# Kernel tuning notes

Measured on AMD Instinct MI355X. Metric: run time of the kernel, lower is better.

Reference implementation:

```python
import jax, jax.numpy as jnp
import numpy as np

# Scaled-up constants (GRID_SIZE=96)
AFFINE_HIDDEN_DIM = 128
ATTENTION_DIM = 256
EMBEDDING_DIM = 512
MAX_CONTRAST = 1.8
RANGE_SIZE = 4
NUM_RANGE_BLOCKS = 13824   # (96//4)**3
NUM_DOMAIN_BLOCKS = 1728   # (96//8)**3
SOFTMAX_TEMPERATURE = 0.25


def setup_inputs() -> dict:
    key = jax.random.key(0)
    ks = jax.random.split(key, 17)
    E, A, H = EMBEDDING_DIM, ATTENTION_DIM, AFFINE_HIDDEN_DIM
    NR, ND = NUM_RANGE_BLOCKS, NUM_DOMAIN_BLOCKS
    s_lin = 1.0 / np.sqrt(E)  # torch Linear default init scale
    return {
        "pooled_domains": jax.random.normal(ks[0], (ND, RANGE_SIZE, RANGE_SIZE, RANGE_SIZE), jnp.float32),
        "range_latents": jax.random.normal(ks[1], (NR, E), jnp.float32),
        "domain_latents": jax.random.normal(ks[2], (ND, E), jnp.float32),
        "range_positional": jax.random.normal(ks[3], (NR, E), jnp.float32),
        "domain_positional": jax.random.normal(ks[4], (ND, E), jnp.float32),
        "W_rproj": jax.random.normal(ks[5], (E, A), jnp.float32) * s_lin,
        "b_rproj": jax.random.normal(ks[6], (A,), jnp.float32) * s_lin,
        "W_dproj": jax.random.normal(ks[7], (E, A), jnp.float32) * s_lin,
        "b_dproj": jax.random.normal(ks[8], (A,), jnp.float32) * s_lin,
        "W_rcon": jax.random.normal(ks[9], (E, H), jnp.float32) * s_lin,
        "b_rcon": jax.random.normal(ks[10], (H,), jnp.float32) * s_lin,
        "W_dcon": jax.random.normal(ks[11], (E, H), jnp.float32) * s_lin,
        "b_dcon": jax.random.normal(ks[12], (H,), jnp.float32) * s_lin,
        "W_roff": jax.random.normal(ks[13], (E, H), jnp.float32) * s_lin,
        "b_roff": jax.random.normal(ks[14], (H,), jnp.float32) * s_lin,
        "W_doff": jax.random.normal(ks[15], (E, H), jnp.float32) * s_lin,
        "b_doff": jax.random.normal(ks[16], (H,), jnp.float32) * s_lin,
    }


def reference(pooled_domains, range_latents, domain_latents,
              range_positional, domain_positional,
              W_rproj, b_rproj, W_dproj, b_dproj,
              W_rcon, b_rcon, W_dcon, b_dcon,
              W_roff, b_roff, W_doff, b_doff):
    range_base = range_latents + range_positional      # [NR, E]
    domain_base = domain_latents + domain_positional   # [ND, E]

    range_repr = range_base @ W_rproj + b_rproj        # [NR, A]
    domain_repr = domain_base @ W_dproj + b_dproj      # [ND, A]

    inv_sqrt_h = 1.0 / np.sqrt(AFFINE_HIDDEN_DIM).astype(np.float32)
    range_con = range_base @ W_rcon + b_rcon           # [NR, H]
    domain_con = domain_base @ W_dcon + b_dcon         # [ND, H]
    contrast = jnp.tanh((range_con @ domain_con.T) * inv_sqrt_h) * MAX_CONTRAST  # [NR, ND]

    range_off = range_base @ W_roff + b_roff
    domain_off = domain_base @ W_doff + b_doff
    offset = jnp.tanh((range_off @ domain_off.T) * inv_sqrt_h)  # [NR, ND]

    scale = 1.0 / (np.sqrt(ATTENTION_DIM).astype(np.float32) * SOFTMAX_TEMPERATURE)
    logits = (range_repr @ domain_repr.T) * scale      # [NR, ND]
    weights = jax.nn.softmax(logits, axis=-1)          # [NR, ND]

    domain_flat = pooled_domains.reshape(NUM_DOMAIN_BLOCKS, -1)   # [ND, 64]
    scaled_domains = (weights * contrast) @ domain_flat           # [NR, 64]
    offset_effective = jnp.sum(weights * offset, axis=1, keepdims=True)  # [NR, 1]
    decoded = (scaled_domains + offset_effective).reshape(-1, RANGE_SIZE, RANGE_SIZE, RANGE_SIZE)
    return decoded
```

## Files before the change

### kernel.cpp

```cpp
#include <hip/hip_runtime.h>
#include <stdint.h>

#define NRB 13824
#define NDB 1728
#define EDIM 512
#define SPLIT 18
#define DPB (NDB/SPLIT)
#define TILES (DPB/32)

typedef __attribute__((ext_vector_type(8))) _Float16 h8;
typedef __attribute__((ext_vector_type(4))) float f4;

typedef __attribute__((address_space(3))) void lds_void;
typedef const __attribute__((address_space(1))) void gbl_void;

#define MFMA(a,b,c) __builtin_amdgcn_mfma_f32_16x16x32_f16(a,b,c,0,0,0)

static __device__ __forceinline__ ushort f2h(float f){
  union { _Float16 h; ushort u; } cv;
  cv.h = (_Float16)f;
  return cv.u;
}

static __device__ __forceinline__ float tanh_fast(float x){
  float ax = __builtin_fabsf(x);
  float t = __builtin_amdgcn_exp2f(ax * -2.8853900817779268f);
  float r = (1.0f - t) * __builtin_amdgcn_rcpf(1.0f + t);
  return __builtin_copysignf(r, x);
}

__global__ void prep_kernel(
    const float* __restrict__ pooled,
    const float* __restrict__ rlat, const float* __restrict__ dlat,
    const float* __restrict__ rpos, const float* __restrict__ dpos,
    const float* __restrict__ Wrp, const float* __restrict__ brp,
    const float* __restrict__ Wdp, const float* __restrict__ bdp,
    const float* __restrict__ Wrc, const float* __restrict__ brc,
    const float* __restrict__ Wdc, const float* __restrict__ bdc,
    const float* __restrict__ Wro, const float* __restrict__ bro,
    const float* __restrict__ Wdo2, const float* __restrict__ bdo2,
    ushort* __restrict__ rb, ushort* __restrict__ db,
    ushort* __restrict__ Wr_t, ushort* __restrict__ Wd_t,
    float* __restrict__ br_c, float* __restrict__ bd_c,
    ushort* __restrict__ dflt)
{
  const int NRE = NRB*EDIM, NDE = NDB*EDIM;
  int i0 = blockIdx.x*blockDim.x + threadIdx.x;
  int stride = gridDim.x*blockDim.x;
  for (int i=i0; i<NRE; i+=stride) rb[i] = f2h(rlat[i]+rpos[i]);
  for (int i=i0; i<NDE; i+=stride) db[i] = f2h(dlat[i]+dpos[i]);
  for (int i=i0; i<512*512; i+=stride){
    int n = i>>9, k = i&511;
    float vr = (n<256) ? Wrp[k*256+n] : ((n<384) ? Wrc[k*128+(n-256)] : Wro[k*128+(n-384)]);
    float vd = (n<256) ? Wdp[k*256+n] : ((n<384) ? Wdc[k*128+(n-256)] : Wdo2[k*128+(n-384)]);
    Wr_t[i] = f2h(vr); Wd_t[i] = f2h(vd);
  }
  for (int i=i0; i<512; i+=stride){
    br_c[i] = (i<256) ? brp[i] : ((i<384) ? brc[i-256] : bro[i-384]);
    bd_c[i] = (i<256) ? bdp[i] : ((i<384) ? bdc[i-256] : bdo2[i-384]);
  }
  for (int i=i0; i<64*NDB; i+=stride){
    int c = i/NDB, d = i - c*NDB;
    dflt[i] = f2h(pooled[d*64+c]);
  }
}

__global__ __launch_bounds__(256) void gemm_feats(
    const ushort* __restrict__ A,
    const ushort* __restrict__ Bt,
    const float* __restrict__ bias,
    ushort* __restrict__ C,
    int M)
{
  __shared__ ushort As[128*32];
  __shared__ ushort Bs[128*32];
  const int tid = threadIdx.x;
  const int lane = tid & 63;
  const int wave = tid >> 6;
  const int l15 = lane & 15;
  const int lhi = lane >> 4;
  const int row0 = blockIdx.x * 128;
  const int col0 = blockIdx.y * 128;
  const int wr = (wave>>1)*64;
  const int wc = (wave&1)*64;

  f4 acc[4][4] = {};
  char* Ab = (char*)As; char* Bb = (char*)Bs;

  for (int k0=0; k0<EDIM; k0+=32){
    __syncthreads();
    #pragma unroll
    for (int c=0;c<2;c++){
      int L = (tid + c*256)*16;
      int r = L>>6;
      int kb = L&63;
      int kbs = kb ^ ((r&3)<<4);
      int ra = row0 + r; if (ra > M-1) ra = M-1;
      const ushort* srcA = A + (size_t)ra*EDIM + k0 + (kbs>>1);
      const ushort* srcB = Bt + (size_t)(col0+r)*EDIM + k0 + (kbs>>1);
      __builtin_amdgcn_global_load_lds((gbl_void*)srcA, (lds_void*)(Ab + L), 16, 0, 0);
      __builtin_amdgcn_global_load_lds((gbl_void*)srcB, (lds_void*)(Bb + L), 16, 0, 0);
    }
    __syncthreads();
    h8 af[4], bf[4];
    #pragma unroll
    for (int i=0;i<4;i++){
      int rowa = wr + i*16 + l15;
      af[i] = *(const h8*)(Ab + (((rowa*64) + lhi*16) ^ ((rowa&3)<<4)));
      int rowb = wc + i*16 + l15;
      bf[i] = *(const h8*)(Bb + (((rowb*64) + lhi*16) ^ ((rowb&3)<<4)));
    }
    #pragma unroll
    for (int i=0;i<4;i++){
      #pragma unroll
      for (int j=0;j<4;j++){
        acc[i][j] = MFMA(af[i], bf[j], acc[i][j]);
      }
    }
  }

  #pragma unroll
  for (int j=0;j<4;j++){
    int col = col0 + wc + j*16 + l15;
    float bv = bias[col];
    #pragma unroll
    for (int i=0;i<4;i++){
      #pragma unroll
      for (int r=0;r<4;r++){
        int row = row0 + wr + i*16 + lhi*4 + r;
        if (row < M) C[(size_t)row*EDIM + col] = f2h(acc[i][j][r] + bv);
      }
    }
  }
}

__global__ __launch_bounds__(512, 2) void attn_kernel(
    const ushort* __restrict__ rfeat,
    const ushort* __restrict__ dfeat,
    const ushort* __restrict__ dflt,
    ushort* __restrict__ accbuf,
    float* __restrict__ mlbuf)
{
  __shared__ ushort DF[DPB*512];
  __shared__ ushort PT[8][16*32];

  const int tid  = threadIdx.x;
  const int wave = tid >> 6;
  const int lane = tid & 63;
  const int l15  = lane & 15;
  const int lhi  = lane >> 4;
  const int wrow = blockIdx.x*128 + wave*16;
  const int by   = blockIdx.y;
  const int dbase = by * DPB;

  constexpr float CL = 0.25f * 1.4426950408889634f;
  constexpr float CH = 0.08838834764831845f;

  char* DFb = (char*)DF;
  char* PTb = (char*)PT[wave];

  #pragma unroll
  for (int c=0;c<12;c++){
    int id = tid + c*512;
    int dom = id >> 6;
    h8 v = *(const h8*)(dfeat + (size_t)(dbase+dom)*EDIM + (id&63)*8);
    *(h8*)(DFb + ((id*16) ^ ((dom&7)<<4))) = v;
  }

  h8 q[16];
  {
    const ushort* qr = rfeat + (size_t)(wrow + l15)*EDIM + lhi*8;
    #pragma unroll
    for (int c=0;c<16;c++) q[c] = *(const h8*)(qr + c*32);
  }

  f4 acc[4] = {};
  float m2[4], lsum[4] = {0.f,0.f,0.f,0.f}, offa[4] = {0.f,0.f,0.f,0.f};
  #pragma unroll
  for (int r=0;r<4;r++) m2[r] = -1e30f;

  __syncthreads();

  for (int t=0; t<TILES; ++t){
    const int d0 = dbase + t*32;
    const int dloc = t*32;

    f4 SL[2] = {}, SC[2] = {}, SO[2] = {};
    #pragma unroll
    for (int ct=0; ct<2; ++ct){
      const int dom = dloc + ct*16 + l15;
      const int swz = (dom&7)<<4;
      const int base = dom*1024 + lhi*16;
      #pragma unroll
      for (int c=0;c<8;c++){
        h8 b = *(const h8*)(DFb + ((base + c*64) ^ swz));
        SL[ct] = MFMA(q[c], b, SL[ct]);
      }
      #pragma unroll
      for (int c=8;c<12;c++){
        h8 b = *(const h8*)(DFb + ((base + c*64) ^ swz));
        SC[ct] = MFMA(q[c], b, SC[ct]);
      }
      #pragma unroll
      for (int c=12;c<16;c++){
        h8 b = *(const h8*)(DFb + ((base + c*64) ^ swz));
        SO[ct] = MFMA(q[c], b, SO[ct]);
      }
    }

    #pragma unroll
    for (int r=0;r<4;r++){
      float la = SL[0][r]*CL;
      float lb = SL[1][r]*CL;
      float tm = fmaxf(la, lb);
      tm = fmaxf(tm, __shfl_xor(tm, 1, 64));
      tm = fmaxf(tm, __shfl_xor(tm, 2, 64));
      tm = fmaxf(tm, __shfl_xor(tm, 4, 64));
      tm = fmaxf(tm, __shfl_xor(tm, 8, 64));
      float mn = fmaxf(m2[r], tm);
      float al = __builtin_amdgcn_exp2f(m2[r] - mn);
      m2[r] = mn;
      lsum[r] *= al; offa[r] *= al;
      acc[0][r] *= al; acc[1][r] *= al; acc[2][r] *= al; acc[3][r] *= al;
      float pa = __builtin_amdgcn_exp2f(la - mn);
      float pb = __builtin_amdgcn_exp2f(lb - mn);
      lsum[r] += pa + pb;
      float ca = tanh_fast(SC[0][r]*CH)*1.8f;
      float cb = tanh_fast(SC[1][r]*CH)*1.8f;
      float oa = tanh_fast(SO[0][r]*CH);
      float ob = tanh_fast(SO[1][r]*CH);
      offa[r] += pa*oa + pb*ob;
      int row = lhi*4 + r;
      int rswz = (row&3)<<4;
      *(ushort*)(PTb + ((row*64 + l15*2) ^ rswz))      = f2h(pa*ca);
      *(ushort*)(PTb + ((row*64 + 32 + l15*2) ^ rswz)) = f2h(pb*cb);
    }

    __builtin_amdgcn_sched_barrier(0);

    {
      h8 pa = *(const h8*)(PTb + ((l15*64 + lhi*16) ^ ((l15&3)<<4)));
      #pragma unroll
      for (int nt=0; nt<4; nt++){
        int n = nt*16 + l15;
        h8 vb = *(const h8*)(dflt + (size_t)n*NDB + d0 + lhi*8);
        acc[nt] = MFMA(pa, vb, acc[nt]);
      }
    }

    __builtin_amdgcn_sched_barrier(0);
  }

  #pragma unroll
  for (int r=0;r<4;r++){
    float ls = lsum[r], oa = offa[r];
    ls += __shfl_xor(ls,1,64); ls += __shfl_xor(ls,2,64);
    ls += __shfl_xor(ls,4,64); ls += __shfl_xor(ls,8,64);
    oa += __shfl_xor(oa,1,64); oa += __shfl_xor(oa,2,64);
    oa += __shfl_xor(oa,4,64); oa += __shfl_xor(oa,8,64);
    int row = wrow + lhi*4 + r;
    size_t base = ((size_t)by*NRB + row)*64;
    #pragma unroll
    for (int nt=0; nt<4; nt++){
      accbuf[base + nt*16 + l15] = f2h(acc[nt][r]);
    }
    if (l15 == 0){
      size_t mo = ((size_t)by*NRB + row)*4;
      mlbuf[mo+0] = m2[r];
      mlbuf[mo+1] = ls;
      mlbuf[mo+2] = oa;
    }
  }
}

__global__ __launch_bounds__(256) void combine_kernel(
    const ushort* __restrict__ accbuf,
    const float* __restrict__ mlbuf,
    float* __restrict__ out)
{
  __shared__ float wS[64][SPLIT];
  __shared__ float c0S[64], iTS[64];
  const int rb = blockIdx.x;
  const int tid = threadIdx.x;

  if (tid < 64){
    int row = rb*64 + tid;
    float M = -1e30f;
    float m[SPLIT], l[SPLIT], o[SPLIT];
    #pragma unroll
    for (int s=0;s<SPLIT;s++){
      size_t off = ((size_t)s*NRB + row)*4;
      m[s]=mlbuf[off]; l[s]=mlbuf[off+1]; o[s]=mlbuf[off+2];
      M = fmaxf(M, m[s]);
    }
    float T=0.f, C=0.f;
    #pragma unroll
    for (int s=0;s<SPLIT;s++){
      float w = __builtin_amdgcn_exp2f(m[s]-M);
      wS[tid][s]=w; T += l[s]*w; C += o[s]*w;
    }
    c0S[tid]=C; iTS[tid]=1.0f/T;
  }
  __syncthreads();

  const int row_l = tid>>2;
  const int cb = (tid&3)*16;
  const int row = rb*64 + row_l;
  float res[16] = {};
  #pragma unroll
  for (int s=0;s<SPLIT;s++){
    float w = wS[row_l][s];
    const ushort* ap = accbuf + ((size_t)s*NRB + row)*64 + cb;
    h8 v0 = *(const h8*)(ap);
    h8 v1 = *(const h8*)(ap + 8);
    #pragma unroll
    for (int j=0;j<8;j++){
      res[j]   += (float)v0[j]*w;
      res[j+8] += (float)v1[j]*w;
    }
  }
  float C = c0S[row_l], iT = iTS[row_l];
  #pragma unroll
  for (int j=0;j<16;j++) out[(size_t)row*64 + cb + j] = (res[j]+C)*iT;
}

extern "C" void kernel_launch(void* const* d_in, const int* in_sizes, int n_in,
                              void* d_out, int out_size, void* d_ws, size_t ws_size,
                              hipStream_t stream) {
  const float* pooled = (const float*)d_in[0];
  const float* rlat   = (const float*)d_in[1];
  const float* dlat   = (const float*)d_in[2];
  const float* rpos   = (const float*)d_in[3];
  const float* dpos   = (const float*)d_in[4];
  const float* Wrp    = (const float*)d_in[5];
  const float* brp    = (const float*)d_in[6];
  const float* Wdp    = (const float*)d_in[7];
  const float* bdp    = (const float*)d_in[8];
  const float* Wrc    = (const float*)d_in[9];
  const float* brc    = (const float*)d_in[10];
  const float* Wdc    = (const float*)d_in[11];
  const float* bdc    = (const float*)d_in[12];
  const float* Wro    = (const float*)d_in[13];
  const float* bro    = (const float*)d_in[14];
  const float* Wdo2   = (const float*)d_in[15];
  const float* bdo2   = (const float*)d_in[16];

  char* ws = (char*)d_ws;
  size_t off = 0;
  ushort* rb    = (ushort*)(ws + off); off += (size_t)NRB*EDIM*2;
  ushort* db    = (ushort*)(ws + off); off += (size_t)NDB*EDIM*2;
  ushort* Wr_t  = (ushort*)(ws + off); off += (size_t)512*512*2;
  ushort* Wd_t  = (ushort*)(ws + off); off += (size_t)512*512*2;
  float*  br_c  = (float*)(ws + off);  off += 512*4;
  float*  bd_c  = (float*)(ws + off);  off += 512*4;
  ushort* rfeat = (ushort*)(ws + off); off += (size_t)NRB*EDIM*2;
  ushort* dfeat = (ushort*)(ws + off); off += (size_t)NDB*EDIM*2;
  ushort* dflt  = (ushort*)(ws + off); off += (size_t)64*NDB*2;
  ushort* accb  = (ushort*)(ws + off); off += (size_t)SPLIT*NRB*64*2;
  float*  mlb   = (float*)(ws + off);  off += (size_t)SPLIT*NRB*4*4;

  prep_kernel<<<2048, 256, 0, stream>>>(pooled, rlat, dlat, rpos, dpos,
      Wrp, brp, Wdp, bdp, Wrc, brc, Wdc, bdc, Wro, bro, Wdo2, bdo2,
      rb, db, Wr_t, Wd_t, br_c, bd_c, dflt);

  gemm_feats<<<dim3(108,4), 256, 0, stream>>>(rb, Wr_t, br_c, rfeat, NRB);
  gemm_feats<<<dim3(14,4),  256, 0, stream>>>(db, Wd_t, bd_c, dfeat, NDB);

  attn_kernel<<<dim3(108, SPLIT), 512, 0, stream>>>(rfeat, dfeat, dflt, accb, mlb);
  combine_kernel<<<216, 256, 0, stream>>>(accb, mlb, (float*)d_out);
}
```

Before: 160.8 us.

## Transpose score MFMAs so each lane owns one row, cutting softmax shuffles

Swaps the MFMA operand order for the score tiles so the output is transposed: each lane now holds four domain columns of a single range row. The per-row max then needs only two cross-lane shuffles instead of four shuffles per register, and running max/sum/offset become scalars. P values are written to LDS as packed 4-wide vector stores. The accumulator rescale factors are fetched with extra lane shuffles so they match the PV accumulator layout. In exchange the LDS write pattern changes, and the swizzle may now produce bank conflicts.

```diff
diff --git a/kernel.cpp b/kernel.cpp
--- a/kernel.cpp
+++ b/kernel.cpp
@@ -10,6 +10,7 @@
 
 typedef __attribute__((ext_vector_type(8))) _Float16 h8;
 typedef __attribute__((ext_vector_type(4))) float f4;
+typedef __attribute__((ext_vector_type(4))) unsigned short us4;
 
 typedef __attribute__((address_space(3))) void lds_void;
 typedef const __attribute__((address_space(1))) void gbl_void;
@@ -175,9 +176,8 @@
   }
 
   f4 acc[4] = {};
-  float m2[4], lsum[4] = {0.f,0.f,0.f,0.f}, offa[4] = {0.f,0.f,0.f,0.f};
-  #pragma unroll
-  for (int r=0;r<4;r++) m2[r] = -1e30f;
+  float m = -1e30f, lsum = 0.f, offa = 0.f;
+  const int sb = (lane & 48) + ((lane >> 4) << 2);
 
   __syncthreads();
 
@@ -194,51 +194,62 @@
       #pragma unroll
       for (int c=0;c<8;c++){
         h8 b = *(const h8*)(DFb + ((base + c*64) ^ swz));
-        SL[ct] = MFMA(q[c], b, SL[ct]);
+        SL[ct] = MFMA(b, q[c], SL[ct]);
       }
       #pragma unroll
       for (int c=8;c<12;c++){
         h8 b = *(const h8*)(DFb + ((base + c*64) ^ swz));
-        SC[ct] = MFMA(q[c], b, SC[ct]);
+        SC[ct] = MFMA(b, q[c], SC[ct]);
       }
       #pragma unroll
       for (int c=12;c<16;c++){
         h8 b = *(const h8*)(DFb + ((base + c*64) ^ swz));
-        SO[ct] = MFMA(q[c], b, SO[ct]);
-      }
-    }
-
+        SO[ct] = MFMA(b, q[c], SO[ct]);
+      }
+    }
+
+    float lm = fmaxf(
+        fmaxf(fmaxf(SL[0][0],SL[0][1]), fmaxf(SL[0][2],SL[0][3])),
+        fmaxf(fmaxf(SL[1][0],SL[1][1]), fmaxf(SL[1][2],SL[1][3]))) * CL;
+    lm = fmaxf(lm, __shfl_xor(lm, 16, 64));
+    lm = fmaxf(lm, __shfl_xor(lm, 32, 64));
+    float mn = fmaxf(m, lm);
+    float al = __builtin_amdgcn_exp2f(m - mn);
+    m = mn;
+    lsum *= al; offa *= al;
+
+    us4 w0, w1;
     #pragma unroll
     for (int r=0;r<4;r++){
-      float la = SL[0][r]*CL;
-      float lb = SL[1][r]*CL;
-      float tm = fmaxf(la, lb);
-      tm = fmaxf(tm, __shfl_xor(tm, 1, 64));
-      tm = fmaxf(tm, __shfl_xor(tm, 2, 64));
-      tm = fmaxf(tm, __shfl_xor(tm, 4, 64));
-      tm = fmaxf(tm, __shfl_xor(tm, 8, 64));
-      float mn = fmaxf(m2[r], tm);
-      float al = __builtin_amdgcn_exp2f(m2[r] - mn);
-      m2[r] = mn;
-      lsum[r] *= al; offa[r] *= al;
-      acc[0][r] *= al; acc[1][r] *= al; acc[2][r] *= al; acc[3][r] *= al;
-      float pa = __builtin_amdgcn_exp2f(la - mn);
-      float pb = __builtin_amdgcn_exp2f(lb - mn);
-      lsum[r] += pa + pb;
-      float ca = tanh_fast(SC[0][r]*CH)*1.8f;
-      float cb = tanh_fast(SC[1][r]*CH)*1.8f;
-      float oa = tanh_fast(SO[0][r]*CH);
-      float ob = tanh_fast(SO[1][r]*CH);
-      offa[r] += pa*oa + pb*ob;
-      int row = lhi*4 + r;
-      int rswz = (row&3)<<4;
-      *(ushort*)(PTb + ((row*64 + l15*2) ^ rswz))      = f2h(pa*ca);
-      *(ushort*)(PTb + ((row*64 + 32 + l15*2) ^ rswz)) = f2h(pb*cb);
+      float p0 = __builtin_amdgcn_exp2f(SL[0][r]*CL - mn);
+      float p1 = __builtin_amdgcn_exp2f(SL[1][r]*CL - mn);
+      lsum += p0 + p1;
+      float c0 = tanh_fast(SC[0][r]*CH)*1.8f;
+      float c1 = tanh_fast(SC[1][r]*CH)*1.8f;
+      float o0 = tanh_fast(SO[0][r]*CH);
+      float o1 = tanh_fast(SO[1][r]*CH);
+      offa += p0*o0 + p1*o1;
+      w0[r] = f2h(p0*c0);
+      w1[r] = f2h(p1*c1);
+    }
+    {
+      const int wbase = l15*64;
+      const int xs = (l15&3)<<4;
+      *(us4*)(PTb + ((wbase + lhi*8) ^ xs))      = w0;
+      *(us4*)(PTb + ((wbase + 32 + lhi*8) ^ xs)) = w1;
     }
 
     __builtin_amdgcn_sched_barrier(0);
 
     {
+      float alr[4];
+      #pragma unroll
+      for (int r=0;r<4;r++) alr[r] = __shfl(al, sb + r, 64);
+      #pragma unroll
+      for (int nt=0; nt<4; nt++){
+        acc[nt][0]*=alr[0]; acc[nt][1]*=alr[1];
+        acc[nt][2]*=alr[2]; acc[nt][3]*=alr[3];
+      }
       h8 pa = *(const h8*)(PTb + ((l15*64 + lhi*16) ^ ((l15&3)<<4)));
       #pragma unroll
       for (int nt=0; nt<4; nt++){
@@ -251,25 +262,24 @@
     __builtin_amdgcn_sched_barrier(0);
   }
 
+  float ls = lsum, oa = offa;
+  ls += __shfl_xor(ls, 16, 64); ls += __shfl_xor(ls, 32, 64);
+  oa += __shfl_xor(oa, 16, 64); oa += __shfl_xor(oa, 32, 64);
+
   #pragma unroll
   for (int r=0;r<4;r++){
-    float ls = lsum[r], oa = offa[r];
-    ls += __shfl_xor(ls,1,64); ls += __shfl_xor(ls,2,64);
-    ls += __shfl_xor(ls,4,64); ls += __shfl_xor(ls,8,64);
-    oa += __shfl_xor(oa,1,64); oa += __shfl_xor(oa,2,64);
-    oa += __shfl_xor(oa,4,64); oa += __shfl_xor(oa,8,64);
     int row = wrow + lhi*4 + r;
     size_t base = ((size_t)by*NRB + row)*64;
     #pragma unroll
     for (int nt=0; nt<4; nt++){
       accbuf[base + nt*16 + l15] = f2h(acc[nt][r]);
     }
-    if (l15 == 0){
-      size_t mo = ((size_t)by*NRB + row)*4;
-      mlbuf[mo+0] = m2[r];
-      mlbuf[mo+1] = ls;
-      mlbuf[mo+2] = oa;
-    }
+  }
+  if (lane < 16){
+    size_t mo = ((size_t)by*NRB + wrow + l15)*4;
+    mlbuf[mo+0] = m;
+    mlbuf[mo+1] = ls;
+    mlbuf[mo+2] = oa;
   }
 }
 
```

Measured after the change: 150.6 us. 6.3% less time.
